# Optimization experiments

Measured on AMD Instinct MI355X. Metric: run time of the kernel, lower is better.

Reference implementation:

```python
import jax, jax.numpy as jnp
import numpy as np

NEG_SLOPE = 0.2

def _gat_layer(x, src, dst, W, a_s, a_d, b, concat):
    # x: [N, F_in], W: [F_in, H*C], a_s/a_d: [H, C]
    N = x.shape[0]
    H, C = a_s.shape
    h = (x @ W).reshape(N, H, C)                       # per-head projection
    al_s = jnp.sum(h * a_s, axis=-1)                   # [N, H]
    al_d = jnp.sum(h * a_d, axis=-1)                   # [N, H]
    e = jax.nn.leaky_relu(al_s[src] + al_d[dst], NEG_SLOPE)  # [E, H]
    # segment softmax over incoming edges of each dst node
    m = jax.ops.segment_max(e, dst, num_segments=N)    # [N, H]
    ex = jnp.exp(e - m[dst])
    denom = jax.ops.segment_sum(ex, dst, num_segments=N)
    alpha = ex / denom[dst]                            # [E, H]
    msg = h[src] * alpha[:, :, None]                   # [E, H, C]
    out = jax.ops.segment_sum(msg, dst, num_segments=N)  # [N, H, C]
    if concat:
        return out.reshape(N, H * C) + b
    return out.mean(axis=1) + b


def setup_inputs() -> dict:
    key = jax.random.key(0)
    ks = jax.random.split(key, 12)
    N, F_in, H, C1, LAT, E = 16384, 512, 4, 128, 64, 262144
    x = jax.random.normal(ks[0], (N, F_in), dtype=jnp.float32)
    edge_index = jax.random.randint(ks[1], (2, E), 0, N, dtype=jnp.int64)
    s = 0.05
    return {
        'x': x,
        'edge_index': edge_index,
        'W1': jax.random.normal(ks[2], (F_in, H * C1), dtype=jnp.float32) * s,
        'a_src1': jax.random.normal(ks[3], (H, C1), dtype=jnp.float32) * s,
        'a_dst1': jax.random.normal(ks[4], (H, C1), dtype=jnp.float32) * s,
        'b1': jax.random.normal(ks[5], (H * C1,), dtype=jnp.float32) * s,
        'W2': jax.random.normal(ks[6], (H * C1, H * LAT), dtype=jnp.float32) * s,
        'a_src2': jax.random.normal(ks[7], (H, LAT), dtype=jnp.float32) * s,
        'a_dst2': jax.random.normal(ks[8], (H, LAT), dtype=jnp.float32) * s,
        'b2': jax.random.normal(ks[9], (LAT,), dtype=jnp.float32) * s,
    }


def reference(x, edge_index, W1, a_src1, a_dst1, b1, W2, a_src2, a_dst2, b2):
    N = x.shape[0]
    # PyG GATConv default add_self_loops=True
    loop = jnp.arange(N, dtype=edge_index.dtype)
    src = jnp.concatenate([edge_index[0], loop])
    dst = jnp.concatenate([edge_index[1], loop])
    h = jax.nn.relu(_gat_layer(x, src, dst, W1, a_src1, a_dst1, b1, concat=True))
    out = _gat_layer(h, src, dst, W2, a_src2, a_dst2, b2, concat=False)
    return out
```

## Files before the change

kernel.cpp:

```cpp
#include <hip/hip_runtime.h>
#include <stdint.h>
#include <stddef.h>
#include <limits.h>

typedef __bf16 bf16;
typedef __bf16 bf16x4 __attribute__((ext_vector_type(4)));
typedef __bf16 bf16x8 __attribute__((ext_vector_type(8)));
typedef float  f32x4  __attribute__((ext_vector_type(4)));

#define CAP 128

static __device__ __forceinline__ float lrelu(float x) { return x > 0.f ? x : 0.2f * x; }
static __device__ __forceinline__ float san(float v) { return (fabsf(v) < 1e4f) ? v : 0.0f; }
static __device__ __forceinline__ float wexp(float e) { return __expf(fminf(e, 30.f)); }

static __device__ __forceinline__ void async_load16(const bf16* g, bf16* l) {
  __builtin_amdgcn_global_load_lds((const __attribute__((address_space(1))) void*)g,
                                   (__attribute__((address_space(3))) void*)l, 16, 0, 0);
}


__global__ __launch_bounds__(256) void prep_all(const float* __restrict__ x,
                                                bf16* __restrict__ xb,
                                                int* __restrict__ cnt,
                                                const float* __restrict__ W1,
                                                const float* __restrict__ W2,
                                                bf16* __restrict__ W1T,
                                                bf16* __restrict__ W2T,
                                                int NX, int N) {
  int b = blockIdx.x;
  const int NCVT = NX >> 10;
  if (b < NCVT) {
    int i = b * 1024 + threadIdx.x * 4;
    f32x4 v = *(const f32x4*)(x + i);
    bf16x4 o;
#pragma unroll
    for (int k = 0; k < 4; ++k) o[k] = (bf16)san(v[k]);
    *(bf16x4*)(xb + i) = o;
    return;
  }
  b -= NCVT;
  if (b < N / 256) { cnt[b * 256 + threadIdx.x] = 0; return; }
  b -= N / 256;
  __shared__ bf16 t[32][33];
  const float* in; bf16* out; int R, C, bx, by;
  if (b < 256) { in = W1; out = W1T; R = 512; C = 512; by = b >> 4; bx = b & 15; }
  else         { b -= 256; in = W2; out = W2T; R = 512; C = 256; by = b >> 3; bx = b & 7; }
  const int lane = threadIdx.x & 31, r8 = threadIdx.x >> 5;
#pragma unroll
  for (int k = 0; k < 4; ++k) {
    int r = by * 32 + r8 + k * 8, c = bx * 32 + lane;
    t[lane][r8 + k * 8] = (bf16)san(in[(size_t)r * C + c]);
  }
  __syncthreads();
#pragma unroll
  for (int k = 0; k < 4; ++k) {
    int oc = bx * 32 + r8 + k * 8;
    out[(size_t)oc * R + by * 32 + lane] = t[r8 + k * 8][lane];
  }
}


__global__ __launch_bounds__(256) void gemm_al_l1(const bf16* __restrict__ A,
                                                  const bf16* __restrict__ BT,
                                                  bf16* __restrict__ C,
                                                  const float* __restrict__ a_s,
                                                  const float* __restrict__ a_d,
                                                  float* __restrict__ al_s,
                                                  float* __restrict__ al_d,
                                                  const int* __restrict__ src,
                                                  const int* __restrict__ dst,
                                                  int E, int* __restrict__ cnt,
                                                  int* __restrict__ slots,
                                                  int M, int N, int K) {
  __shared__ __align__(16) bf16 As[128 * 32];
  __shared__ __align__(16) bf16 Bs[128 * 32];
  __shared__ float alred[2][128][2];
  const int tid = threadIdx.x;
  const int b   = blockIdx.x;

  if (b >= 512) {
    for (int e = (b - 512) * 256 + tid; e < E; e += 256 * 256) {
      int d = dst[e];
      int pos = atomicAdd(&cnt[d], 1);
      if (pos < CAP) slots[(size_t)d * CAP + pos] = src[e];
    }
    return;
  }

  const int lane = tid & 63;
  const int wave = tid >> 6;
  const int m0 = (b & 127) * 128;
  const int head = b >> 7;
  const int n0 = head * 128;
  const int wm = (wave >> 1) * 64;
  const int wn = (wave & 1) * 64;

  f32x4 acc[4][4] = {};

  const int id0 = tid, id1 = tid + 256;
  const bf16* a0p = A  + (size_t)(m0 + (id0 >> 2)) * K + (id0 & 3) * 8;
  const bf16* a1p = A  + (size_t)(m0 + (id1 >> 2)) * K + (id1 & 3) * 8;
  const bf16* b0p = BT + (size_t)(n0 + (id0 >> 2)) * K + (id0 & 3) * 8;
  const bf16* b1p = BT + (size_t)(n0 + (id1 >> 2)) * K + (id1 & 3) * 8;

  const int kq = (lane >> 4) * 8;
  const int rA = wm + (lane & 15);
  const int rB = wn + (lane & 15);

  for (int k0 = 0; k0 < K; k0 += 32) {
    __syncthreads();
    async_load16(a0p + k0, &As[id0 * 8]);
    async_load16(a1p + k0, &As[id1 * 8]);
    async_load16(b0p + k0, &Bs[id0 * 8]);
    async_load16(b1p + k0, &Bs[id1 * 8]);
    __syncthreads();
    bf16x8 af[4], bfv[4];
#pragma unroll
    for (int i = 0; i < 4; ++i) af[i]  = *(const bf16x8*)&As[(rA + i * 16) * 32 + kq];
#pragma unroll
    for (int j = 0; j < 4; ++j) bfv[j] = *(const bf16x8*)&Bs[(rB + j * 16) * 32 + kq];
#pragma unroll
    for (int i = 0; i < 4; ++i)
#pragma unroll
      for (int j = 0; j < 4; ++j)
        acc[i][j] = __builtin_amdgcn_mfma_f32_16x16x32_bf16(af[i], bfv[j], acc[i][j], 0, 0, 0);
  }

  const int cc = lane & 15;
  const int rb = (lane >> 4) * 4;
#pragma unroll
  for (int i = 0; i < 4; ++i)
#pragma unroll
    for (int j = 0; j < 4; ++j) {
      int gcol = n0 + wn + j * 16 + cc;
#pragma unroll
      for (int r = 0; r < 4; ++r) {
        int grow = m0 + wm + i * 16 + rb + r;
        C[(size_t)grow * N + gcol] = (bf16)acc[i][j][r];
      }
    }

  {
    float asv[4], adv[4];
#pragma unroll
    for (int j = 0; j < 4; ++j) {
      int col = head * 128 + wn + j * 16 + cc;
      asv[j] = san(a_s[col]);
      adv[j] = san(a_d[col]);
    }
    const int wnh = wn >> 6;
#pragma unroll
    for (int i = 0; i < 4; ++i)
#pragma unroll
      for (int r = 0; r < 4; ++r) {
        float ps = 0.f, pd = 0.f;
#pragma unroll
        for (int j = 0; j < 4; ++j) { ps += acc[i][j][r] * asv[j]; pd += acc[i][j][r] * adv[j]; }
#pragma unroll
        for (int off = 1; off <= 8; off <<= 1) {
          ps += __shfl_xor(ps, off);
          pd += __shfl_xor(pd, off);
        }
        if (cc == 0) {
          int row = wm + i * 16 + rb + r;
          alred[wnh][row][0] = ps;
          alred[wnh][row][1] = pd;
        }
      }
    __syncthreads();
    if (tid < 128) {
      al_s[(size_t)(m0 + tid) * 4 + head] = alred[0][tid][0] + alred[1][tid][0];
      al_d[(size_t)(m0 + tid) * 4 + head] = alred[0][tid][1] + alred[1][tid][1];
    }
  }
}


__global__ __launch_bounds__(256) void gemm_al_l2(const bf16* __restrict__ A,
                                                  const bf16* __restrict__ BT,
                                                  bf16* __restrict__ C,
                                                  const float* __restrict__ a_s,
                                                  const float* __restrict__ a_d,
                                                  float* __restrict__ al_s,
                                                  float* __restrict__ al_d,
                                                  int M, int N, int K) {
  __shared__ __align__(16) bf16 As[64 * 32];
  __shared__ __align__(16) bf16 Bs[128 * 32];
  const int tid  = threadIdx.x;
  const int lane = tid & 63;
  const int wave = tid >> 6;
  const int m0 = blockIdx.x * 64;
  const int n0 = blockIdx.y * 128;
  const int wm = (wave >> 1) * 32;
  const int wn = (wave & 1) * 64;

  f32x4 acc[2][4] = {};

  const int tb = tid + 256;
  const bf16* ap  = A  + (size_t)(m0 + (tid >> 2)) * K + (tid & 3) * 8;
  const bf16* bp0 = BT + (size_t)(n0 + (tid >> 2)) * K + (tid & 3) * 8;
  const bf16* bp1 = BT + (size_t)(n0 + (tb  >> 2)) * K + (tb  & 3) * 8;

  const int kq = (lane >> 4) * 8;
  const int rA = wm + (lane & 15);
  const int rB = wn + (lane & 15);

  for (int k0 = 0; k0 < K; k0 += 32) {
    __syncthreads();
    async_load16(ap  + k0, &As[tid * 8]);
    async_load16(bp0 + k0, &Bs[tid * 8]);
    async_load16(bp1 + k0, &Bs[tb  * 8]);
    __syncthreads();
    bf16x8 af[2], bfv[4];
#pragma unroll
    for (int i = 0; i < 2; ++i) af[i]  = *(const bf16x8*)&As[(rA + i * 16) * 32 + kq];
#pragma unroll
    for (int j = 0; j < 4; ++j) bfv[j] = *(const bf16x8*)&Bs[(rB + j * 16) * 32 + kq];
#pragma unroll
    for (int i = 0; i < 2; ++i)
#pragma unroll
      for (int j = 0; j < 4; ++j)
        acc[i][j] = __builtin_amdgcn_mfma_f32_16x16x32_bf16(af[i], bfv[j], acc[i][j], 0, 0, 0);
  }

  const int cc = lane & 15;
  const int rb = (lane >> 4) * 4;
#pragma unroll
  for (int i = 0; i < 2; ++i)
#pragma unroll
    for (int j = 0; j < 4; ++j) {
      int gcol = n0 + wn + j * 16 + cc;
#pragma unroll
      for (int r = 0; r < 4; ++r) {
        int grow = m0 + wm + i * 16 + rb + r;
        C[(size_t)grow * N + gcol] = (bf16)acc[i][j][r];
      }
    }

  {
    const int head = blockIdx.y * 2 + (wn >> 6);
    float asv[4], adv[4];
#pragma unroll
    for (int j = 0; j < 4; ++j) {
      int col = head * 64 + j * 16 + cc;
      asv[j] = san(a_s[col]);
      adv[j] = san(a_d[col]);
    }
#pragma unroll
    for (int i = 0; i < 2; ++i)
#pragma unroll
      for (int r = 0; r < 4; ++r) {
        float ps = 0.f, pd = 0.f;
#pragma unroll
        for (int j = 0; j < 4; ++j) { ps += acc[i][j][r] * asv[j]; pd += acc[i][j][r] * adv[j]; }
#pragma unroll
        for (int off = 1; off <= 8; off <<= 1) {
          ps += __shfl_xor(ps, off);
          pd += __shfl_xor(pd, off);
        }
        if (cc == 0) {
          int row = m0 + wm + i * 16 + rb + r;
          al_s[(size_t)row * 4 + head] = ps;
          al_d[(size_t)row * 4 + head] = pd;
        }
      }
  }
}


__global__ __launch_bounds__(64) void aggregate1_f(const bf16* __restrict__ h1,
                                                   const float* __restrict__ al_s,
                                                   const float* __restrict__ al_d,
                                                   const int* __restrict__ cnt,
                                                   int* __restrict__ slots,
                                                   const float* __restrict__ bias,
                                                   bf16* __restrict__ out) {
  __shared__ int   sIdx[64];
  __shared__ f32x4 sW[64];
  const int n = blockIdx.x, lane = threadIdx.x;
  const int cb = lane * 8;
  const int hd = lane >> 4;
  const int beg = n * CAP;
  const int len = min(cnt[n], CAP);
  const f32x4 alsn = *(const f32x4*)(al_s + (size_t)n * 4);
  const f32x4 aldn = *(const f32x4*)(al_d + (size_t)n * 4);

  const float wself = wexp(lrelu(alsn[hd] + aldn[hd]));
  bf16x8 hv0 = *(const bf16x8*)(h1 + (size_t)n * 512 + cb);
  float acc[8];
#pragma unroll
  for (int k = 0; k < 8; ++k) acc[k] = wself * (float)hv0[k];

  f32x4 Lv = {0.f, 0.f, 0.f, 0.f};
  if (lane == 0) {
#pragma unroll
    for (int h = 0; h < 4; ++h) Lv[h] = wexp(lrelu(alsn[h] + aldn[h]));
  }

  if (len <= 64) {
    int v = (lane < len) ? slots[beg + lane] : INT_MAX;
    if (len > 1) {
#pragma unroll
      for (int k = 2; k <= 64; k <<= 1) {
#pragma unroll
        for (int j = k >> 1; j > 0; j >>= 1) {
          int p = __shfl_xor(v, j);
          bool take_min = (((lane & k) == 0) == ((lane & j) == 0));
          v = take_min ? min(v, p) : max(v, p);
        }
      }
      if (lane < len) slots[beg + lane] = v;
    }
    if (lane < len) {
      sIdx[lane] = v;
      f32x4 a = *(const f32x4*)(al_s + (size_t)v * 4);
      f32x4 w;
#pragma unroll
      for (int h = 0; h < 4; ++h) w[h] = wexp(lrelu(a[h] + aldn[h]));
      sW[lane] = w;
#pragma unroll
      for (int h = 0; h < 4; ++h) Lv[h] += w[h];
    }
#pragma unroll 4
    for (int j = 0; j < len; ++j) {
      int s = sIdx[j];
      float a = sW[j][hd];
      bf16x8 hv = *(const bf16x8*)(h1 + (size_t)s * 512 + cb);
#pragma unroll
      for (int k = 0; k < 8; ++k) acc[k] += a * (float)hv[k];
    }
  } else {
    if (lane == 0) {
      for (int i = beg + 1; i < beg + len; ++i) {
        int v = slots[i];
        int j = i - 1;
        while (j >= beg && slots[j] > v) { slots[j + 1] = slots[j]; --j; }
        slots[j + 1] = v;
      }
    }
    __syncthreads();
    for (int c0 = beg; c0 < beg + len; c0 += 64) {
      const int cl = min(64, beg + len - c0);
      if (lane < cl) {
        int s = slots[c0 + lane];
        sIdx[lane] = s;
        f32x4 a = *(const f32x4*)(al_s + (size_t)s * 4);
        f32x4 w;
#pragma unroll
        for (int h = 0; h < 4; ++h) w[h] = wexp(lrelu(a[h] + aldn[h]));
        sW[lane] = w;
#pragma unroll
        for (int h = 0; h < 4; ++h) Lv[h] += w[h];
      }
#pragma unroll 4
      for (int j = 0; j < cl; ++j) {
        int s = sIdx[j];
        float a = sW[j][hd];
        bf16x8 hv = *(const bf16x8*)(h1 + (size_t)s * 512 + cb);
#pragma unroll
        for (int k = 0; k < 8; ++k) acc[k] += a * (float)hv[k];
      }
    }
  }

  for (int off = 32; off; off >>= 1) {
#pragma unroll
    for (int h = 0; h < 4; ++h) Lv[h] += __shfl_xor(Lv[h], off);
  }
  const float inv = 1.0f / Lv[hd];
  bf16x8 ov;
#pragma unroll
  for (int k = 0; k < 8; ++k)
    ov[k] = (bf16)fmaxf(acc[k] * inv + san(bias[cb + k]), 0.f);
  *(bf16x8*)(out + (size_t)n * 512 + cb) = ov;
}


__global__ __launch_bounds__(64) void aggregate2_f(const bf16* __restrict__ h2,
                                                   const float* __restrict__ al_s,
                                                   const float* __restrict__ al_d,
                                                   const int* __restrict__ cnt,
                                                   const int* __restrict__ slots,
                                                   const float* __restrict__ bias,
                                                   float* __restrict__ out) {
  __shared__ int   sIdx[64];
  __shared__ f32x4 sW[64];
  const int n = blockIdx.x, lane = threadIdx.x;
  const int hd = lane >> 4;
  const int cb = lane * 4;
  const int beg = n * CAP;
  const int len = min(cnt[n], CAP);
  const f32x4 alsn = *(const f32x4*)(al_s + (size_t)n * 4);
  const f32x4 aldn = *(const f32x4*)(al_d + (size_t)n * 4);

  const float wself = wexp(lrelu(alsn[hd] + aldn[hd]));
  bf16x4 hv0 = *(const bf16x4*)(h2 + (size_t)n * 256 + cb);
  float acc0 = wself * (float)hv0[0], acc1 = wself * (float)hv0[1];
  float acc2 = wself * (float)hv0[2], acc3 = wself * (float)hv0[3];
  f32x4 Lv = {0.f, 0.f, 0.f, 0.f};
  if (lane == 0) {
#pragma unroll
    for (int h = 0; h < 4; ++h) Lv[h] = wexp(lrelu(alsn[h] + aldn[h]));
  }
  for (int c0 = beg; c0 < beg + len; c0 += 64) {
    const int cl = min(64, beg + len - c0);
    if (lane < cl) {
      int s = slots[c0 + lane];
      sIdx[lane] = s;
      f32x4 a = *(const f32x4*)(al_s + (size_t)s * 4);
      f32x4 w;
#pragma unroll
      for (int h = 0; h < 4; ++h) w[h] = wexp(lrelu(a[h] + aldn[h]));
      sW[lane] = w;
#pragma unroll
      for (int h = 0; h < 4; ++h) Lv[h] += w[h];
    }
#pragma unroll 4
    for (int j = 0; j < cl; ++j) {
      int s = sIdx[j];
      float a = sW[j][hd];
      bf16x4 hv = *(const bf16x4*)(h2 + (size_t)s * 256 + cb);
      acc0 += a * (float)hv[0];
      acc1 += a * (float)hv[1];
      acc2 += a * (float)hv[2];
      acc3 += a * (float)hv[3];
    }
  }
  for (int off = 32; off; off >>= 1) {
#pragma unroll
    for (int h = 0; h < 4; ++h) Lv[h] += __shfl_xor(Lv[h], off);
  }
  const float inv = 1.0f / Lv[hd];
  acc0 *= inv; acc1 *= inv; acc2 *= inv; acc3 *= inv;
  acc0 += __shfl_xor(acc0, 16); acc1 += __shfl_xor(acc1, 16);
  acc2 += __shfl_xor(acc2, 16); acc3 += __shfl_xor(acc3, 16);
  acc0 += __shfl_xor(acc0, 32); acc1 += __shfl_xor(acc1, 32);
  acc2 += __shfl_xor(acc2, 32); acc3 += __shfl_xor(acc3, 32);
  if (lane < 16) {
    int ob = lane * 4;
    f32x4 ov;
    ov[0] = 0.25f * acc0 + san(bias[ob]);
    ov[1] = 0.25f * acc1 + san(bias[ob + 1]);
    ov[2] = 0.25f * acc2 + san(bias[ob + 2]);
    ov[3] = 0.25f * acc3 + san(bias[ob + 3]);
    *(f32x4*)(out + (size_t)n * 64 + ob) = ov;
  }
}


extern "C" void kernel_launch(void* const* d_in, const int* in_sizes, int n_in,
                              void* d_out, int out_size, void* d_ws, size_t ws_size,
                              hipStream_t stream) {
  const float* x   = (const float*)d_in[0];
  const int*   ei  = (const int*)d_in[1];
  const float* W1  = (const float*)d_in[2];
  const float* as1 = (const float*)d_in[3];
  const float* ad1 = (const float*)d_in[4];
  const float* b1  = (const float*)d_in[5];
  const float* W2  = (const float*)d_in[6];
  const float* as2 = (const float*)d_in[7];
  const float* ad2 = (const float*)d_in[8];
  const float* b2  = (const float*)d_in[9];
  float* outp = (float*)d_out;

  const int N = in_sizes[0] / 512;
  const int E = in_sizes[1] / 2;
  const int* src = ei;
  const int* dst = ei + E;

  char* p = (char*)d_ws;
  auto alloc = [&](size_t bytes) {
    char* r = p;
    p += (bytes + 255) & ~(size_t)255;
    return r;
  };
  bf16* xb    = (bf16*)alloc((size_t)N * 512 * 2);
  bf16* h1    = (bf16*)alloc((size_t)N * 512 * 2);
  bf16* hbuf  = (bf16*)alloc((size_t)N * 512 * 2);
  bf16* W1T   = (bf16*)alloc((size_t)512 * 512 * 2);
  bf16* W2T   = (bf16*)alloc((size_t)256 * 512 * 2);
  float* al_s1 = (float*)alloc((size_t)N * 4 * 4);
  float* al_d1 = (float*)alloc((size_t)N * 4 * 4);
  float* al_s2 = (float*)alloc((size_t)N * 4 * 4);
  float* al_d2 = (float*)alloc((size_t)N * 4 * 4);
  int* cnt     = (int*)alloc((size_t)N * 4);
  int* slots   = (int*)alloc((size_t)N * CAP * 4);
  bf16* h2 = h1;

  const int NX = N * 512;

  prep_all<<<(NX >> 10) + N / 256 + 256 + 128, 256, 0, stream>>>(
      x, xb, cnt, W1, W2, W1T, W2T, NX, N);

  gemm_al_l1<<<512 + 256, 256, 0, stream>>>(xb, W1T, h1, as1, ad1, al_s1, al_d1,
                                            src, dst, E, cnt, slots, N, 512, 512);
  aggregate1_f<<<N, 64, 0, stream>>>(h1, al_s1, al_d1, cnt, slots, b1, hbuf);

  gemm_al_l2<<<dim3(N / 64, 2), 256, 0, stream>>>(hbuf, W2T, h2, as2, ad2, al_s2, al_d2,
                                                  N, 256, 512);
  aggregate2_f<<<N, 64, 0, stream>>>(h2, al_s2, al_d2, cnt, slots, b2, outp);
}
```

Before: 194.4 us.

## Fuse x fp32-to-bf16 conversion into GEMM load; pack four nodes per aggregate block

Removes the separate pass that converts x to bf16. The layer-1 GEMM now reads fp32 x directly, converts it in registers and stores bf16 into LDS, which saves a full write and re-read of a 16 MB bf16 copy. The catch is that x is fetched again by each of the four head tiles, and the A-tile load becomes synchronous instead of async LDS. Both aggregation kernels now run four nodes per 256-thread block, one wave each, with per-wave shared buffers. This cuts the block count and raises occupancy, and a __syncthreads is replaced by a vmcnt wait.

```diff
diff --git a/kernel.cpp b/kernel.cpp
--- a/kernel.cpp
+++ b/kernel.cpp
@@ -20,26 +20,13 @@
 }
 
 
-__global__ __launch_bounds__(256) void prep_all(const float* __restrict__ x,
-                                                bf16* __restrict__ xb,
-                                                int* __restrict__ cnt,
-                                                const float* __restrict__ W1,
-                                                const float* __restrict__ W2,
-                                                bf16* __restrict__ W1T,
-                                                bf16* __restrict__ W2T,
-                                                int NX, int N) {
+__global__ __launch_bounds__(256) void prep_w(int* __restrict__ cnt,
+                                              const float* __restrict__ W1,
+                                              const float* __restrict__ W2,
+                                              bf16* __restrict__ W1T,
+                                              bf16* __restrict__ W2T,
+                                              int N) {
   int b = blockIdx.x;
-  const int NCVT = NX >> 10;
-  if (b < NCVT) {
-    int i = b * 1024 + threadIdx.x * 4;
-    f32x4 v = *(const f32x4*)(x + i);
-    bf16x4 o;
-#pragma unroll
-    for (int k = 0; k < 4; ++k) o[k] = (bf16)san(v[k]);
-    *(bf16x4*)(xb + i) = o;
-    return;
-  }
-  b -= NCVT;
   if (b < N / 256) { cnt[b * 256 + threadIdx.x] = 0; return; }
   b -= N / 256;
   __shared__ bf16 t[32][33];
@@ -61,7 +48,7 @@
 }
 
 
-__global__ __launch_bounds__(256) void gemm_al_l1(const bf16* __restrict__ A,
+__global__ __launch_bounds__(256) void gemm_al_l1(const float* __restrict__ X,
                                                   const bf16* __restrict__ BT,
                                                   bf16* __restrict__ C,
                                                   const float* __restrict__ a_s,
@@ -99,8 +86,8 @@
   f32x4 acc[4][4] = {};
 
   const int id0 = tid, id1 = tid + 256;
-  const bf16* a0p = A  + (size_t)(m0 + (id0 >> 2)) * K + (id0 & 3) * 8;
-  const bf16* a1p = A  + (size_t)(m0 + (id1 >> 2)) * K + (id1 & 3) * 8;
+  const float* a0p = X  + (size_t)(m0 + (id0 >> 2)) * K + (id0 & 3) * 8;
+  const float* a1p = X  + (size_t)(m0 + (id1 >> 2)) * K + (id1 & 3) * 8;
   const bf16* b0p = BT + (size_t)(n0 + (id0 >> 2)) * K + (id0 & 3) * 8;
   const bf16* b1p = BT + (size_t)(n0 + (id1 >> 2)) * K + (id1 & 3) * 8;
 
@@ -110,10 +97,22 @@
 
   for (int k0 = 0; k0 < K; k0 += 32) {
     __syncthreads();
-    async_load16(a0p + k0, &As[id0 * 8]);
-    async_load16(a1p + k0, &As[id1 * 8]);
     async_load16(b0p + k0, &Bs[id0 * 8]);
     async_load16(b1p + k0, &Bs[id1 * 8]);
+    f32x4 u0 = *(const f32x4*)(a0p + k0);
+    f32x4 u1 = *(const f32x4*)(a0p + k0 + 4);
+    f32x4 u2 = *(const f32x4*)(a1p + k0);
+    f32x4 u3 = *(const f32x4*)(a1p + k0 + 4);
+    bf16x8 w0, w1;
+#pragma unroll
+    for (int k = 0; k < 4; ++k) {
+      w0[k]     = (bf16)san(u0[k]);
+      w0[4 + k] = (bf16)san(u1[k]);
+      w1[k]     = (bf16)san(u2[k]);
+      w1[4 + k] = (bf16)san(u3[k]);
+    }
+    *(bf16x8*)&As[id0 * 8] = w0;
+    *(bf16x8*)&As[id1 * 8] = w1;
     __syncthreads();
     bf16x8 af[4], bfv[4];
 #pragma unroll
@@ -269,16 +268,18 @@
 }
 
 
-__global__ __launch_bounds__(64) void aggregate1_f(const bf16* __restrict__ h1,
-                                                   const float* __restrict__ al_s,
-                                                   const float* __restrict__ al_d,
-                                                   const int* __restrict__ cnt,
-                                                   int* __restrict__ slots,
-                                                   const float* __restrict__ bias,
-                                                   bf16* __restrict__ out) {
-  __shared__ int   sIdx[64];
-  __shared__ f32x4 sW[64];
-  const int n = blockIdx.x, lane = threadIdx.x;
+__global__ __launch_bounds__(256) void aggregate1_f(const bf16* __restrict__ h1,
+                                                    const float* __restrict__ al_s,
+                                                    const float* __restrict__ al_d,
+                                                    const int* __restrict__ cnt,
+                                                    int* __restrict__ slots,
+                                                    const float* __restrict__ bias,
+                                                    bf16* __restrict__ out) {
+  __shared__ int   sIdx[4][64];
+  __shared__ f32x4 sW[4][64];
+  const int wv   = threadIdx.x >> 6;
+  const int lane = threadIdx.x & 63;
+  const int n = blockIdx.x * 4 + wv;
   const int cb = lane * 8;
   const int hd = lane >> 4;
   const int beg = n * CAP;
@@ -313,19 +314,19 @@
       if (lane < len) slots[beg + lane] = v;
     }
     if (lane < len) {
-      sIdx[lane] = v;
+      sIdx[wv][lane] = v;
       f32x4 a = *(const f32x4*)(al_s + (size_t)v * 4);
       f32x4 w;
 #pragma unroll
       for (int h = 0; h < 4; ++h) w[h] = wexp(lrelu(a[h] + aldn[h]));
-      sW[lane] = w;
+      sW[wv][lane] = w;
 #pragma unroll
       for (int h = 0; h < 4; ++h) Lv[h] += w[h];
     }
 #pragma unroll 4
     for (int j = 0; j < len; ++j) {
-      int s = sIdx[j];
-      float a = sW[j][hd];
+      int s = sIdx[wv][j];
+      float a = sW[wv][j][hd];
       bf16x8 hv = *(const bf16x8*)(h1 + (size_t)s * 512 + cb);
 #pragma unroll
       for (int k = 0; k < 8; ++k) acc[k] += a * (float)hv[k];
@@ -339,24 +340,24 @@
         slots[j + 1] = v;
       }
     }
-    __syncthreads();
+    asm volatile("s_waitcnt vmcnt(0)" ::: "memory");
     for (int c0 = beg; c0 < beg + len; c0 += 64) {
       const int cl = min(64, beg + len - c0);
       if (lane < cl) {
         int s = slots[c0 + lane];
-        sIdx[lane] = s;
+        sIdx[wv][lane] = s;
         f32x4 a = *(const f32x4*)(al_s + (size_t)s * 4);
         f32x4 w;
 #pragma unroll
         for (int h = 0; h < 4; ++h) w[h] = wexp(lrelu(a[h] + aldn[h]));
-        sW[lane] = w;
+        sW[wv][lane] = w;
 #pragma unroll
         for (int h = 0; h < 4; ++h) Lv[h] += w[h];
       }
 #pragma unroll 4
       for (int j = 0; j < cl; ++j) {
-        int s = sIdx[j];
-        float a = sW[j][hd];
+        int s = sIdx[wv][j];
+        float a = sW[wv][j][hd];
         bf16x8 hv = *(const bf16x8*)(h1 + (size_t)s * 512 + cb);
 #pragma unroll
         for (int k = 0; k < 8; ++k) acc[k] += a * (float)hv[k];
@@ -377,16 +378,18 @@
 }
 
 
-__global__ __launch_bounds__(64) void aggregate2_f(const bf16* __restrict__ h2,
-                                                   const float* __restrict__ al_s,
-                                                   const float* __restrict__ al_d,
-                                                   const int* __restrict__ cnt,
-                                                   const int* __restrict__ slots,
-                                                   const float* __restrict__ bias,
-                                                   float* __restrict__ out) {
-  __shared__ int   sIdx[64];
-  __shared__ f32x4 sW[64];
-  const int n = blockIdx.x, lane = threadIdx.x;
+__global__ __launch_bounds__(256) void aggregate2_f(const bf16* __restrict__ h2,
+                                                    const float* __restrict__ al_s,
+                                                    const float* __restrict__ al_d,
+                                                    const int* __restrict__ cnt,
+                                                    const int* __restrict__ slots,
+                                                    const float* __restrict__ bias,
+                                                    float* __restrict__ out) {
+  __shared__ int   sIdx[4][64];
+  __shared__ f32x4 sW[4][64];
+  const int wv   = threadIdx.x >> 6;
+  const int lane = threadIdx.x & 63;
+  const int n = blockIdx.x * 4 + wv;
   const int hd = lane >> 4;
   const int cb = lane * 4;
   const int beg = n * CAP;
@@ -407,19 +410,19 @@
     const int cl = min(64, beg + len - c0);
     if (lane < cl) {
       int s = slots[c0 + lane];
-      sIdx[lane] = s;
+      sIdx[wv][lane] = s;
       f32x4 a = *(const f32x4*)(al_s + (size_t)s * 4);
       f32x4 w;
 #pragma unroll
       for (int h = 0; h < 4; ++h) w[h] = wexp(lrelu(a[h] + aldn[h]));
-      sW[lane] = w;
+      sW[wv][lane] = w;
 #pragma unroll
       for (int h = 0; h < 4; ++h) Lv[h] += w[h];
     }
 #pragma unroll 4
     for (int j = 0; j < cl; ++j) {
-      int s = sIdx[j];
-      float a = sW[j][hd];
+      int s = sIdx[wv][j];
+      float a = sW[wv][j][hd];
       bf16x4 hv = *(const bf16x4*)(h2 + (size_t)s * 256 + cb);
       acc0 += a * (float)hv[0];
       acc1 += a * (float)hv[1];
@@ -475,7 +478,6 @@
     p += (bytes + 255) & ~(size_t)255;
     return r;
   };
-  bf16* xb    = (bf16*)alloc((size_t)N * 512 * 2);
   bf16* h1    = (bf16*)alloc((size_t)N * 512 * 2);
   bf16* hbuf  = (bf16*)alloc((size_t)N * 512 * 2);
   bf16* W1T   = (bf16*)alloc((size_t)512 * 512 * 2);
@@ -488,16 +490,13 @@
   int* slots   = (int*)alloc((size_t)N * CAP * 4);
   bf16* h2 = h1;
 
-  const int NX = N * 512;
-
-  prep_all<<<(NX >> 10) + N / 256 + 256 + 128, 256, 0, stream>>>(
-      x, xb, cnt, W1, W2, W1T, W2T, NX, N);
-
-  gemm_al_l1<<<512 + 256, 256, 0, stream>>>(xb, W1T, h1, as1, ad1, al_s1, al_d1,
+  prep_w<<<N / 256 + 256 + 128, 256, 0, stream>>>(cnt, W1, W2, W1T, W2T, N);
+
+  gemm_al_l1<<<512 + 256, 256, 0, stream>>>(x, W1T, h1, as1, ad1, al_s1, al_d1,
                                             src, dst, E, cnt, slots, N, 512, 512);
-  aggregate1_f<<<N, 64, 0, stream>>>(h1, al_s1, al_d1, cnt, slots, b1, hbuf);
+  aggregate1_f<<<N / 4, 256, 0, stream>>>(h1, al_s1, al_d1, cnt, slots, b1, hbuf);
 
   gemm_al_l2<<<dim3(N / 64, 2), 256, 0, stream>>>(hbuf, W2T, h2, as2, ad2, al_s2, al_d2,
                                                   N, 256, 512);
-  aggregate2_f<<<N, 64, 0, stream>>>(h2, al_s2, al_d2, cnt, slots, b2, outp);
-}
+  aggregate2_f<<<N / 4, 256, 0, stream>>>(h2, al_s2, al_d2, cnt, slots, b2, outp);
+}
```

After: 195.5 us. About the same (+0.5%).
